# Kernel tuning notes

Measured on AMD Instinct MI355X. Metric: run time of the kernel, lower is better.

## Reference

```python
import jax, jax.numpy as jnp
import numpy as np

B, S, P = 256, 1024, 4096   # batch, n_sensors, n_points
NM, H, PD = 64, 128, 128    # n_modes, hidden width, p
C = 1.0                     # speed of light param


def setup_inputs() -> dict:
    key = jax.random.key(0)
    ks = jax.random.split(key, 16)
    w = lambda k, shp: (jax.random.normal(k, shp, jnp.float32) * 0.05)
    return {
        "u0": jax.random.normal(ks[0], (B, S), jnp.float32),
        "x": jax.random.uniform(ks[1], (P,), jnp.float32, -1.0, 1.0),
        "t": jax.random.uniform(ks[2], (P,), jnp.float32, 0.0, 1.0),
        # branch MLP: (2*NM)->128->128->PD
        "bw1": w(ks[3], (H, 2 * NM)), "bb1": jnp.zeros((H,), jnp.float32),
        "bw2": w(ks[4], (H, H)),      "bb2": jnp.zeros((H,), jnp.float32),
        "bw3": w(ks[5], (PD, H)),     "bb3": jnp.zeros((PD,), jnp.float32),
        # trunk MLP: 4->128->128->PD
        "tw1": w(ks[6], (H, 4)),      "tb1": jnp.zeros((H,), jnp.float32),
        "tw2": w(ks[7], (H, H)),      "tb2": jnp.zeros((H,), jnp.float32),
        "tw3": w(ks[8], (PD, H)),     "tb3": jnp.zeros((PD,), jnp.float32),
    }


def _mlp(a, w1, b1, w2, b2, w3, b3):
    a = jax.nn.relu(a @ w1.T + b1)
    a = jax.nn.relu(a @ w2.T + b2)
    return a @ w3.T + b3


def reference(u0, x, t, bw1, bb1, bw2, bb2, bw3, bb3, tw1, tb1, tw2, tb2, tw3, tb3):
    # Fourier coefficients: mean over sensors of u0 * cos/sin(pi*k*xs)
    xs = jnp.linspace(-1.0, 1.0, S, dtype=jnp.float32)          # (S,)
    modes = jnp.arange(1, NM + 1, dtype=jnp.float32)            # (NM,)
    ang = jnp.pi * modes[:, None] * xs[None, :]                 # (NM, S)
    cos_c = (u0 @ jnp.cos(ang).T) / S                           # (B, NM)
    sin_c = (u0 @ jnp.sin(ang).T) / S                           # (B, NM)
    fourier = jnp.concatenate([cos_c, sin_c], axis=1)           # (B, 2*NM)

    branch_out = _mlp(fourier, bw1, bb1, bw2, bb2, bw3, bb3)    # (B, PD)

    xe = jnp.broadcast_to(x[None, :], (u0.shape[0], P))         # (B, P)
    te = jnp.broadcast_to(t[None, :], (u0.shape[0], P))
    pt_sq = te ** 2 - xe ** 2 / (C ** 2)
    # safe sqrt of clamp(pt_sq, min=0)
    proper_time = jnp.sqrt(jnp.where(pt_sq > 0, pt_sq, 0.0) + 0.0)
    causal = (jnp.abs(xe) <= C * te).astype(jnp.float32)
    trunk_feat = jnp.stack([xe, te, proper_time, causal], axis=-1)  # (B, P, 4)

    trunk_out = _mlp(trunk_feat, tw1, tb1, tw2, tb2, tw3, tb3)      # (B, P, PD)

    u_pred = jnp.einsum("bd,bpd->bp", branch_out, trunk_out)        # (B, P)
    return u_pred * causal
```

## Files before the change

kernel.cpp:

```cpp
#include <hip/hip_runtime.h>
#include <hip/hip_fp16.h>
#include <math.h>

#define NMODES 64
#define SDIM   1024
#define BATCH  256
#define PDIM   4096
#define HDIM   128

typedef _Float16 half8 __attribute__((ext_vector_type(8)));
typedef float f32x4 __attribute__((ext_vector_type(4)));

#define WSB_BRANCH 0
#define WSB_T3     (BATCH * HDIM * 2)

__global__ __launch_bounds__(256) void k_fused(
    const float* __restrict__ u0,
    const float* __restrict__ xv, const float* __restrict__ tv,
    const float* __restrict__ bw1, const float* __restrict__ bb1,
    const float* __restrict__ bw2, const float* __restrict__ bb2,
    const float* __restrict__ bw3, const float* __restrict__ bb3,
    const float* __restrict__ tw1, const float* __restrict__ tb1,
    const float* __restrict__ tw2, const float* __restrict__ tb2,
    const float* __restrict__ tw3, const float* __restrict__ tb3,
    __half* __restrict__ branch_out, __half* __restrict__ t3g) {
    __shared__ float h1L[16 * 132];
    __shared__ float h2L[16 * 132];
    __shared__ float featL[16][4];
    __shared__ float u0s[2][SDIM];
    __shared__ float part[2][2][HDIM];
    __shared__ float fr[2][HDIM];
    __shared__ float hh[2][HDIM];

    const int t = threadIdx.x;

    if (blockIdx.x < 256) {
        const int pbase = blockIdx.x * 16;
        const int j = t & 127;
        const int pg = t >> 7;

        if (t < 16) {
            int p = pbase + t;
            float x = xv[p], tt = tv[p];
            float q = tt * tt - x * x;
            float ptime = (q > 0.f) ? sqrtf(q) : 0.f;
            float c = (fabsf(x) <= tt) ? 1.f : 0.f;
            featL[t][0] = x; featL[t][1] = tt; featL[t][2] = ptime; featL[t][3] = c;
        }
        __syncthreads();

        {
            float4 w1 = ((const float4*)tw1)[j];
            float b1 = tb1[j];
            for (int p = pg; p < 16; p += 2) {
                float4 f = *(const float4*)featL[p];
                float v = fmaf(w1.x, f.x, fmaf(w1.y, f.y, fmaf(w1.z, f.z, fmaf(w1.w, f.w, b1))));
                h1L[p * 132 + j] = fmaxf(v, 0.f);
            }
        }
        __syncthreads();

        {
            const float4* wp = (const float4*)(tw2 + (size_t)j * HDIM);
            float bias = tb2[j];
            float acc[8];
#pragma unroll
            for (int q = 0; q < 8; ++q) acc[q] = bias;
            for (int i4 = 0; i4 < 32; ++i4) {
                float4 wv = wp[i4];
#pragma unroll
                for (int q = 0; q < 8; ++q) {
                    float4 hv = *(const float4*)&h1L[(pg + q * 2) * 132 + i4 * 4];
                    acc[q] += wv.x * hv.x + wv.y * hv.y + wv.z * hv.z + wv.w * hv.w;
                }
            }
#pragma unroll
            for (int q = 0; q < 8; ++q) h2L[(pg + q * 2) * 132 + j] = fmaxf(acc[q], 0.f);
        }
        __syncthreads();

        {
            const float4* wp = (const float4*)(tw3 + (size_t)j * HDIM);
            float bias = tb3[j];
            float acc[8];
#pragma unroll
            for (int q = 0; q < 8; ++q) acc[q] = bias;
            for (int i4 = 0; i4 < 32; ++i4) {
                float4 wv = wp[i4];
#pragma unroll
                for (int q = 0; q < 8; ++q) {
                    float4 hv = *(const float4*)&h2L[(pg + q * 2) * 132 + i4 * 4];
                    acc[q] += wv.x * hv.x + wv.y * hv.y + wv.z * hv.z + wv.w * hv.w;
                }
            }
#pragma unroll
            for (int q = 0; q < 8; ++q)
                t3g[(size_t)(pbase + pg + q * 2) * HDIM + j] = __float2half(acc[q]);
        }
        return;
    }

    const int bb = (blockIdx.x - 256) * 2;
    const int j = t & 127;
    const int half = t >> 7;

    {
        int flat0 = t;
        int row0 = flat0 >> 8, c40 = flat0 & 255;
        ((float4*)u0s[row0])[c40] = ((const float4*)(u0 + (size_t)(bb + row0) * SDIM))[c40];
        int flat1 = t + 256;
        int row1 = flat1 >> 8, c41 = flat1 & 255;
        ((float4*)u0s[row1])[c41] = ((const float4*)(u0 + (size_t)(bb + row1) * SDIM))[c41];
    }
    __syncthreads();

    {
        const int kmode = (j & 63) + 1;
        const int s_lo = half * 512;
        float xs0 = -1.0f + 2.0f * (float)s_lo / 1023.0f;
        float a = 0.5f * (float)kmode * xs0;
        a = a - floorf(a);
        const float r = (float)kmode * (1.0f / 1023.0f);
        float a0 = 0.f, a1 = 0.f;
        if (j < 64) {
#pragma unroll 8
            for (int s = s_lo; s < s_lo + 512; ++s) {
                float bas = __builtin_amdgcn_cosf(a);
                a += r; a = a - floorf(a);
                a0 += bas * u0s[0][s];
                a1 += bas * u0s[1][s];
            }
        } else {
#pragma unroll 8
            for (int s = s_lo; s < s_lo + 512; ++s) {
                float bas = __builtin_amdgcn_sinf(a);
                a += r; a = a - floorf(a);
                a0 += bas * u0s[0][s];
                a1 += bas * u0s[1][s];
            }
        }
        part[half][0][j] = a0;
        part[half][1][j] = a1;
    }
    __syncthreads();
    if (t < 128) {
        const float sc = 1.0f / (float)SDIM;
        fr[0][j] = (part[0][0][j] + part[1][0][j]) * sc;
        fr[1][j] = (part[0][1][j] + part[1][1][j]) * sc;
    }
    __syncthreads();

    if (t < 128) {
        {
            const float4* wp = (const float4*)(bw1 + (size_t)j * HDIM);
            float c0 = bb1[j], c1 = c0;
            for (int i4 = 0; i4 < 32; ++i4) {
                float4 wv = wp[i4];
                float4 x0 = *(const float4*)&fr[0][i4 * 4];
                float4 x1 = *(const float4*)&fr[1][i4 * 4];
                c0 += wv.x * x0.x + wv.y * x0.y + wv.z * x0.z + wv.w * x0.w;
                c1 += wv.x * x1.x + wv.y * x1.y + wv.z * x1.z + wv.w * x1.w;
            }
            hh[0][j] = fmaxf(c0, 0.f); hh[1][j] = fmaxf(c1, 0.f);
        }
        __syncthreads();
        {
            const float4* wp = (const float4*)(bw2 + (size_t)j * HDIM);
            float c0 = bb2[j], c1 = c0;
            for (int i4 = 0; i4 < 32; ++i4) {
                float4 wv = wp[i4];
                float4 x0 = *(const float4*)&hh[0][i4 * 4];
                float4 x1 = *(const float4*)&hh[1][i4 * 4];
                c0 += wv.x * x0.x + wv.y * x0.y + wv.z * x0.z + wv.w * x0.w;
                c1 += wv.x * x1.x + wv.y * x1.y + wv.z * x1.z + wv.w * x1.w;
            }
            fr[0][j] = fmaxf(c0, 0.f); fr[1][j] = fmaxf(c1, 0.f);
        }
        __syncthreads();
        {
            const float4* wp = (const float4*)(bw3 + (size_t)j * HDIM);
            float c0 = bb3[j], c1 = c0;
            for (int i4 = 0; i4 < 32; ++i4) {
                float4 wv = wp[i4];
                float4 x0 = *(const float4*)&fr[0][i4 * 4];
                float4 x1 = *(const float4*)&fr[1][i4 * 4];
                c0 += wv.x * x0.x + wv.y * x0.y + wv.z * x0.z + wv.w * x0.w;
                c1 += wv.x * x1.x + wv.y * x1.y + wv.z * x1.z + wv.w * x1.w;
            }
            branch_out[(size_t)(bb + 0) * HDIM + j] = __float2half(c0);
            branch_out[(size_t)(bb + 1) * HDIM + j] = __float2half(c1);
        }
    } else {
        __syncthreads();
        __syncthreads();
    }
}

#define LDH 144
__global__ __launch_bounds__(256) void k_final(
    const __half* __restrict__ br_g, const __half* __restrict__ t3g,
    const float* __restrict__ xv, const float* __restrict__ tv,
    float* __restrict__ out) {
    __shared__ _Float16 brL[64 * LDH];
    __shared__ _Float16 ttL[64 * LDH];
    __shared__ float causL[64];

    const int t = threadIdx.x;
    const int rb = blockIdx.x >> 6;
    const int cb = blockIdx.x & 63;

    if (t < 64) {
        int p = cb * 64 + t;
        float x = xv[p], tt = tv[p];
        causL[t] = (fabsf(x) <= tt) ? 1.f : 0.f;
    }

#pragma unroll
    for (int it = 0; it < 4; ++it) {
        int flat = t + 256 * it;
        int row = flat >> 4, c = flat & 15;
        *(float4*)&brL[row * LDH + c * 8] =
            *(const float4*)&br_g[(size_t)(rb * 64 + row) * HDIM + c * 8];
        *(float4*)&ttL[row * LDH + c * 8] =
            *(const float4*)&t3g[(size_t)(cb * 64 + row) * HDIM + c * 8];
    }
    __syncthreads();

    const int lane = t & 63;
    const int w = t >> 6;
    const int lm = lane & 15;
    const int q = lane >> 4;

    f32x4 acc[4] = {f32x4{0,0,0,0}, f32x4{0,0,0,0}, f32x4{0,0,0,0}, f32x4{0,0,0,0}};

    const _Float16* aBase = &brL[(16 * w + lm) * LDH + q * 8];
#pragma unroll
    for (int ks = 0; ks < 4; ++ks) {
        half8 af = *(const half8*)(aBase + ks * 32);
#pragma unroll
        for (int jt = 0; jt < 4; ++jt) {
            half8 bf = *(const half8*)&ttL[(16 * jt + lm) * LDH + q * 8 + ks * 32];
            acc[jt] = __builtin_amdgcn_mfma_f32_16x16x32_f16(af, bf, acc[jt], 0, 0, 0);
        }
    }

#pragma unroll
    for (int jt = 0; jt < 4; ++jt) {
        int col = cb * 64 + 16 * jt + lm;
        float cz = causL[16 * jt + lm];
#pragma unroll
        for (int e = 0; e < 4; ++e) {
            int row = rb * 64 + 16 * w + q * 4 + e;
            out[(size_t)row * PDIM + col] = acc[jt][e] * cz;
        }
    }
}

extern "C" void kernel_launch(void* const* d_in, const int* in_sizes, int n_in,
                              void* d_out, int out_size, void* d_ws, size_t ws_size,
                              hipStream_t stream) {
    const float* u0  = (const float*)d_in[0];
    const float* xv  = (const float*)d_in[1];
    const float* tv  = (const float*)d_in[2];
    const float* bw1 = (const float*)d_in[3];
    const float* bb1 = (const float*)d_in[4];
    const float* bw2 = (const float*)d_in[5];
    const float* bb2 = (const float*)d_in[6];
    const float* bw3 = (const float*)d_in[7];
    const float* bb3 = (const float*)d_in[8];
    const float* tw1 = (const float*)d_in[9];
    const float* tb1 = (const float*)d_in[10];
    const float* tw2 = (const float*)d_in[11];
    const float* tb2 = (const float*)d_in[12];
    const float* tw3 = (const float*)d_in[13];
    const float* tb3 = (const float*)d_in[14];

    char* wsb = (char*)d_ws;
    __half* branch_out = (__half*)(wsb + WSB_BRANCH);
    __half* t3g        = (__half*)(wsb + WSB_T3);
    float* out = (float*)d_out;

    hipLaunchKernelGGL(k_fused, dim3(384), dim3(256), 0, stream,
                       u0, xv, tv, bw1, bb1, bw2, bb2, bw3, bb3,
                       tw1, tb1, tw2, tb2, tw3, tb3, branch_out, t3g);
    hipLaunchKernelGGL(k_final, dim3(256), dim3(256), 0, stream,
                       branch_out, t3g, xv, tv, out);
}
```

Before: 105.4 us.

## Run trunk MLP hidden layers on fp16 MFMA and rebalance branch blocks

The trunk MLP's 128x128 layers move from scalar fp32 dot products to fp16 MFMA 16x16x32 instructions. Each block stages the weights as fp16 in shared memory and handles 32 points instead of 16, so there are 128 trunk blocks. Branch blocks now take one batch row each instead of two, giving 256 branch blocks, and the Fourier angle is computed directly per step instead of accumulated. The shared-memory padding in k_final also shrinks. The main cost targeted is the FP32 ALU work of the trunk layers, in exchange for lower precision in the hidden activations and weights and a per-block weight-conversion overhead.

New measurement: 103.0 us. -2.3%, faster.

```diff
diff --git a/kernel.cpp b/kernel.cpp
--- a/kernel.cpp
+++ b/kernel.cpp
@@ -8,13 +8,32 @@
 #define PDIM   4096
 #define HDIM   128
 
-typedef _Float16 half8 __attribute__((ext_vector_type(8)));
-typedef float f32x4 __attribute__((ext_vector_type(4)));
+typedef _Float16 half8  __attribute__((ext_vector_type(8)));
+typedef _Float16 half4v __attribute__((ext_vector_type(4)));
+typedef float    f32x4  __attribute__((ext_vector_type(4)));
 
 #define WSB_BRANCH 0
 #define WSB_T3     (BATCH * HDIM * 2)
 
-__global__ __launch_bounds__(256) void k_fused(
+#define LDW 136
+
+union KMixSmem {
+    struct {
+        _Float16 Ws[128 * LDW];
+        _Float16 h1[32 * LDW];
+        _Float16 h2[32 * LDW];
+        float    feat[32][4];
+    } tr;
+    struct {
+        float u0row[SDIM];
+        float part[2][HDIM];
+        float fr[HDIM];
+        float hh[HDIM];
+        float g2[HDIM];
+    } fb;
+};
+
+__global__ __launch_bounds__(256) void k_mix(
     const float* __restrict__ u0,
     const float* __restrict__ xv, const float* __restrict__ tv,
     const float* __restrict__ bw1, const float* __restrict__ bb1,
@@ -24,179 +43,185 @@
     const float* __restrict__ tw2, const float* __restrict__ tb2,
     const float* __restrict__ tw3, const float* __restrict__ tb3,
     __half* __restrict__ branch_out, __half* __restrict__ t3g) {
-    __shared__ float h1L[16 * 132];
-    __shared__ float h2L[16 * 132];
-    __shared__ float featL[16][4];
-    __shared__ float u0s[2][SDIM];
-    __shared__ float part[2][2][HDIM];
-    __shared__ float fr[2][HDIM];
-    __shared__ float hh[2][HDIM];
-
+    __shared__ KMixSmem sm;
     const int t = threadIdx.x;
 
-    if (blockIdx.x < 256) {
-        const int pbase = blockIdx.x * 16;
-        const int j = t & 127;
-        const int pg = t >> 7;
-
-        if (t < 16) {
+    if (blockIdx.x < 128) {
+        const int pbase = blockIdx.x * 32;
+
+#pragma unroll
+        for (int i = 0; i < 16; ++i) {
+            int F = i * 256 + t;
+            float4 wv = ((const float4*)tw2)[F];
+            half4v h; h.x = (_Float16)wv.x; h.y = (_Float16)wv.y;
+            h.z = (_Float16)wv.z; h.w = (_Float16)wv.w;
+            *(half4v*)&sm.tr.Ws[(F >> 5) * LDW + (F & 31) * 4] = h;
+        }
+        if (t < 32) {
             int p = pbase + t;
             float x = xv[p], tt = tv[p];
-            float q = tt * tt - x * x;
-            float ptime = (q > 0.f) ? sqrtf(q) : 0.f;
-            float c = (fabsf(x) <= tt) ? 1.f : 0.f;
-            featL[t][0] = x; featL[t][1] = tt; featL[t][2] = ptime; featL[t][3] = c;
+            float qq = tt * tt - x * x;
+            sm.tr.feat[t][0] = x;
+            sm.tr.feat[t][1] = tt;
+            sm.tr.feat[t][2] = (qq > 0.f) ? sqrtf(qq) : 0.f;
+            sm.tr.feat[t][3] = (fabsf(x) <= tt) ? 1.f : 0.f;
         }
         __syncthreads();
 
+        const int j = t & 127, pg = t >> 7;
         {
             float4 w1 = ((const float4*)tw1)[j];
             float b1 = tb1[j];
-            for (int p = pg; p < 16; p += 2) {
-                float4 f = *(const float4*)featL[p];
-                float v = fmaf(w1.x, f.x, fmaf(w1.y, f.y, fmaf(w1.z, f.z, fmaf(w1.w, f.w, b1))));
-                h1L[p * 132 + j] = fmaxf(v, 0.f);
+#pragma unroll
+            for (int i = 0; i < 16; ++i) {
+                int p = 2 * i + pg;
+                float4 f = *(const float4*)sm.tr.feat[p];
+                float v = fmaf(w1.x, f.x, fmaf(w1.y, f.y,
+                           fmaf(w1.z, f.z, fmaf(w1.w, f.w, b1))));
+                sm.tr.h1[p * LDW + j] = (_Float16)fmaxf(v, 0.f);
             }
         }
         __syncthreads();
 
+        const int lane = t & 63, w = t >> 6;
+        const int lm = lane & 15, q = lane >> 4;
+        const int mt = w & 1, nh = w >> 1;
+
         {
-            const float4* wp = (const float4*)(tw2 + (size_t)j * HDIM);
-            float bias = tb2[j];
-            float acc[8];
-#pragma unroll
-            for (int q = 0; q < 8; ++q) acc[q] = bias;
-            for (int i4 = 0; i4 < 32; ++i4) {
-                float4 wv = wp[i4];
-#pragma unroll
-                for (int q = 0; q < 8; ++q) {
-                    float4 hv = *(const float4*)&h1L[(pg + q * 2) * 132 + i4 * 4];
-                    acc[q] += wv.x * hv.x + wv.y * hv.y + wv.z * hv.z + wv.w * hv.w;
+            f32x4 acc[4] = {f32x4{0,0,0,0}, f32x4{0,0,0,0},
+                            f32x4{0,0,0,0}, f32x4{0,0,0,0}};
+            const _Float16* aB = &sm.tr.h1[(mt * 16 + lm) * LDW + q * 8];
+#pragma unroll
+            for (int ks = 0; ks < 4; ++ks) {
+                half8 af = *(const half8*)(aB + ks * 32);
+#pragma unroll
+                for (int n = 0; n < 4; ++n) {
+                    half8 bf = *(const half8*)
+                        &sm.tr.Ws[((nh * 4 + n) * 16 + lm) * LDW + q * 8 + ks * 32];
+                    acc[n] = __builtin_amdgcn_mfma_f32_16x16x32_f16(af, bf, acc[n], 0, 0, 0);
                 }
             }
 #pragma unroll
-            for (int q = 0; q < 8; ++q) h2L[(pg + q * 2) * 132 + j] = fmaxf(acc[q], 0.f);
+            for (int n = 0; n < 4; ++n) {
+                int col = (nh * 4 + n) * 16 + lm;
+                float b = tb2[col];
+#pragma unroll
+                for (int e = 0; e < 4; ++e)
+                    sm.tr.h2[(mt * 16 + q * 4 + e) * LDW + col] =
+                        (_Float16)fmaxf(acc[n][e] + b, 0.f);
+            }
         }
         __syncthreads();
 
+#pragma unroll
+        for (int i = 0; i < 16; ++i) {
+            int F = i * 256 + t;
+            float4 wv = ((const float4*)tw3)[F];
+            half4v h; h.x = (_Float16)wv.x; h.y = (_Float16)wv.y;
+            h.z = (_Float16)wv.z; h.w = (_Float16)wv.w;
+            *(half4v*)&sm.tr.Ws[(F >> 5) * LDW + (F & 31) * 4] = h;
+        }
+        __syncthreads();
+
         {
-            const float4* wp = (const float4*)(tw3 + (size_t)j * HDIM);
-            float bias = tb3[j];
-            float acc[8];
-#pragma unroll
-            for (int q = 0; q < 8; ++q) acc[q] = bias;
-            for (int i4 = 0; i4 < 32; ++i4) {
-                float4 wv = wp[i4];
-#pragma unroll
-                for (int q = 0; q < 8; ++q) {
-                    float4 hv = *(const float4*)&h2L[(pg + q * 2) * 132 + i4 * 4];
-                    acc[q] += wv.x * hv.x + wv.y * hv.y + wv.z * hv.z + wv.w * hv.w;
+            f32x4 acc[4] = {f32x4{0,0,0,0}, f32x4{0,0,0,0},
+                            f32x4{0,0,0,0}, f32x4{0,0,0,0}};
+            const _Float16* aB = &sm.tr.h2[(mt * 16 + lm) * LDW + q * 8];
+#pragma unroll
+            for (int ks = 0; ks < 4; ++ks) {
+                half8 af = *(const half8*)(aB + ks * 32);
+#pragma unroll
+                for (int n = 0; n < 4; ++n) {
+                    half8 bf = *(const half8*)
+                        &sm.tr.Ws[((nh * 4 + n) * 16 + lm) * LDW + q * 8 + ks * 32];
+                    acc[n] = __builtin_amdgcn_mfma_f32_16x16x32_f16(af, bf, acc[n], 0, 0, 0);
                 }
             }
 #pragma unroll
-            for (int q = 0; q < 8; ++q)
-                t3g[(size_t)(pbase + pg + q * 2) * HDIM + j] = __float2half(acc[q]);
+            for (int n = 0; n < 4; ++n) {
+                int col = (nh * 4 + n) * 16 + lm;
+                float b = tb3[col];
+#pragma unroll
+                for (int e = 0; e < 4; ++e) {
+                    int p = pbase + mt * 16 + q * 4 + e;
+                    t3g[(size_t)p * HDIM + col] = __float2half(acc[n][e] + b);
+                }
+            }
         }
         return;
     }
 
-    const int bb = (blockIdx.x - 256) * 2;
-    const int j = t & 127;
-    const int half = t >> 7;
-
-    {
-        int flat0 = t;
-        int row0 = flat0 >> 8, c40 = flat0 & 255;
-        ((float4*)u0s[row0])[c40] = ((const float4*)(u0 + (size_t)(bb + row0) * SDIM))[c40];
-        int flat1 = t + 256;
-        int row1 = flat1 >> 8, c41 = flat1 & 255;
-        ((float4*)u0s[row1])[c41] = ((const float4*)(u0 + (size_t)(bb + row1) * SDIM))[c41];
-    }
-    __syncthreads();
-
+    const int row = blockIdx.x - 128;
+    ((float4*)sm.fb.u0row)[t] = ((const float4*)(u0 + (size_t)row * SDIM))[t];
+    __syncthreads();
+
+    const int j = t & 127, sh = t >> 7;
     {
         const int kmode = (j & 63) + 1;
-        const int s_lo = half * 512;
-        float xs0 = -1.0f + 2.0f * (float)s_lo / 1023.0f;
-        float a = 0.5f * (float)kmode * xs0;
-        a = a - floorf(a);
-        const float r = (float)kmode * (1.0f / 1023.0f);
-        float a0 = 0.f, a1 = 0.f;
+        const float r  = (float)kmode * (1.0f / 1023.0f);
+        const float a0 = -0.5f * (float)kmode;
+        float sf = (float)(sh * 512);
+        const float* up = sm.fb.u0row + sh * 512;
+        float acc = 0.f;
         if (j < 64) {
 #pragma unroll 8
-            for (int s = s_lo; s < s_lo + 512; ++s) {
-                float bas = __builtin_amdgcn_cosf(a);
-                a += r; a = a - floorf(a);
-                a0 += bas * u0s[0][s];
-                a1 += bas * u0s[1][s];
+            for (int s = 0; s < 512; ++s) {
+                float a = fmaf(sf, r, a0);
+                a -= floorf(a);
+                acc = fmaf(__builtin_amdgcn_cosf(a), up[s], acc);
+                sf += 1.0f;
             }
         } else {
 #pragma unroll 8
-            for (int s = s_lo; s < s_lo + 512; ++s) {
-                float bas = __builtin_amdgcn_sinf(a);
-                a += r; a = a - floorf(a);
-                a0 += bas * u0s[0][s];
-                a1 += bas * u0s[1][s];
-            }
-        }
-        part[half][0][j] = a0;
-        part[half][1][j] = a1;
-    }
-    __syncthreads();
+            for (int s = 0; s < 512; ++s) {
+                float a = fmaf(sf, r, a0);
+                a -= floorf(a);
+                acc = fmaf(__builtin_amdgcn_sinf(a), up[s], acc);
+                sf += 1.0f;
+            }
+        }
+        sm.fb.part[sh][j] = acc;
+    }
+    __syncthreads();
+    if (t < 128)
+        sm.fb.fr[j] = (sm.fb.part[0][j] + sm.fb.part[1][j]) * (1.0f / (float)SDIM);
+    __syncthreads();
+
     if (t < 128) {
-        const float sc = 1.0f / (float)SDIM;
-        fr[0][j] = (part[0][0][j] + part[1][0][j]) * sc;
-        fr[1][j] = (part[0][1][j] + part[1][1][j]) * sc;
-    }
-    __syncthreads();
-
+        const float4* wp = (const float4*)(bw1 + (size_t)j * HDIM);
+        float c0 = bb1[j];
+        for (int i4 = 0; i4 < 32; ++i4) {
+            float4 wv = wp[i4];
+            float4 x0 = *(const float4*)&sm.fb.fr[i4 * 4];
+            c0 += wv.x * x0.x + wv.y * x0.y + wv.z * x0.z + wv.w * x0.w;
+        }
+        sm.fb.hh[j] = fmaxf(c0, 0.f);
+    }
+    __syncthreads();
     if (t < 128) {
-        {
-            const float4* wp = (const float4*)(bw1 + (size_t)j * HDIM);
-            float c0 = bb1[j], c1 = c0;
-            for (int i4 = 0; i4 < 32; ++i4) {
-                float4 wv = wp[i4];
-                float4 x0 = *(const float4*)&fr[0][i4 * 4];
-                float4 x1 = *(const float4*)&fr[1][i4 * 4];
-                c0 += wv.x * x0.x + wv.y * x0.y + wv.z * x0.z + wv.w * x0.w;
-                c1 += wv.x * x1.x + wv.y * x1.y + wv.z * x1.z + wv.w * x1.w;
-            }
-            hh[0][j] = fmaxf(c0, 0.f); hh[1][j] = fmaxf(c1, 0.f);
-        }
-        __syncthreads();
-        {
-            const float4* wp = (const float4*)(bw2 + (size_t)j * HDIM);
-            float c0 = bb2[j], c1 = c0;
-            for (int i4 = 0; i4 < 32; ++i4) {
-                float4 wv = wp[i4];
-                float4 x0 = *(const float4*)&hh[0][i4 * 4];
-                float4 x1 = *(const float4*)&hh[1][i4 * 4];
-                c0 += wv.x * x0.x + wv.y * x0.y + wv.z * x0.z + wv.w * x0.w;
-                c1 += wv.x * x1.x + wv.y * x1.y + wv.z * x1.z + wv.w * x1.w;
-            }
-            fr[0][j] = fmaxf(c0, 0.f); fr[1][j] = fmaxf(c1, 0.f);
-        }
-        __syncthreads();
-        {
-            const float4* wp = (const float4*)(bw3 + (size_t)j * HDIM);
-            float c0 = bb3[j], c1 = c0;
-            for (int i4 = 0; i4 < 32; ++i4) {
-                float4 wv = wp[i4];
-                float4 x0 = *(const float4*)&fr[0][i4 * 4];
-                float4 x1 = *(const float4*)&fr[1][i4 * 4];
-                c0 += wv.x * x0.x + wv.y * x0.y + wv.z * x0.z + wv.w * x0.w;
-                c1 += wv.x * x1.x + wv.y * x1.y + wv.z * x1.z + wv.w * x1.w;
-            }
-            branch_out[(size_t)(bb + 0) * HDIM + j] = __float2half(c0);
-            branch_out[(size_t)(bb + 1) * HDIM + j] = __float2half(c1);
-        }
-    } else {
-        __syncthreads();
-        __syncthreads();
+        const float4* wp = (const float4*)(bw2 + (size_t)j * HDIM);
+        float c0 = bb2[j];
+        for (int i4 = 0; i4 < 32; ++i4) {
+            float4 wv = wp[i4];
+            float4 x0 = *(const float4*)&sm.fb.hh[i4 * 4];
+            c0 += wv.x * x0.x + wv.y * x0.y + wv.z * x0.z + wv.w * x0.w;
+        }
+        sm.fb.g2[j] = fmaxf(c0, 0.f);
+    }
+    __syncthreads();
+    if (t < 128) {
+        const float4* wp = (const float4*)(bw3 + (size_t)j * HDIM);
+        float c0 = bb3[j];
+        for (int i4 = 0; i4 < 32; ++i4) {
+            float4 wv = wp[i4];
+            float4 x0 = *(const float4*)&sm.fb.g2[i4 * 4];
+            c0 += wv.x * x0.x + wv.y * x0.y + wv.z * x0.z + wv.w * x0.w;
+        }
+        branch_out[(size_t)row * HDIM + j] = __float2half(c0);
     }
 }
 
-#define LDH 144
+#define LDH 136
 __global__ __launch_bounds__(256) void k_final(
     const __half* __restrict__ br_g, const __half* __restrict__ t3g,
     const float* __restrict__ xv, const float* __restrict__ tv,
@@ -280,7 +305,7 @@
     __half* t3g        = (__half*)(wsb + WSB_T3);
     float* out = (float*)d_out;
 
-    hipLaunchKernelGGL(k_fused, dim3(384), dim3(256), 0, stream,
+    hipLaunchKernelGGL(k_mix, dim3(384), dim3(256), 0, stream,
                        u0, xv, tv, bw1, bb1, bw2, bb2, bw3, bb3,
                        tw1, tb1, tw2, tb2, tw3, tb3, branch_out, t3g);
     hipLaunchKernelGGL(k_final, dim3(256), dim3(256), 0, stream,
```
